# Kernel tuning notes

Measured on AMD Instinct MI355X. Metric: run time of the kernel, lower is better.

The kernel has to match this reference:

```python
import jax, jax.numpy as jnp
import numpy as np
from jax import lax

MAX_DISP = 4  # correlation window radius -> 9x9 = 81 offsets


def setup_inputs() -> dict:
    key = jax.random.key(0)
    k1, k2 = jax.random.split(key)
    B, C, H, W = 4, 256, 128, 128
    x_1 = jax.random.normal(k1, (B, C, H, W), dtype=jnp.float32)
    x_2 = jax.random.normal(k2, (B, C, H, W), dtype=jnp.float32)
    return {"x_1": x_1, "x_2": x_2}


def reference(x_1, x_2):
    # FlowNet-style correlation: for each displacement (dy, dx) in [-4, 4]^2,
    # out[b, (dy+4)*9 + (dx+4), y, x] = mean_c x1[b,c,y,x] * x2[b,c,y+dy,x+dx]
    # with zero padding of x2 (normalized by C, as in the original CUDA kernel).
    B, C, H, W = x_1.shape
    pad = jnp.pad(x_2, ((0, 0), (0, 0), (MAX_DISP, MAX_DISP), (MAX_DISP, MAX_DISP)))
    outs = []
    for dy in range(2 * MAX_DISP + 1):
        for dx in range(2 * MAX_DISP + 1):
            shifted = lax.dynamic_slice(pad, (0, 0, dy, dx), (B, C, H, W))
            outs.append(jnp.mean(x_1 * shifted, axis=1))  # [B, H, W]
    return jnp.stack(outs, axis=1)  # [B, 81, H, W]
```

## Files before the change

### kernel.cpp

```cpp
#include <hip/hip_runtime.h>
#include <stdint.h>


#define MD 4
constexpr int Bc = 4, Cc = 256, Hc = 128, Wc = 128;
constexpr int HW = Hc * Wc;
constexpr int TH = 16, TW = 16;
constexpr int CC = 4;
constexpr int SROWS = 18, SCOLS = 24;
constexpr int X2_SLOTS = CC * SROWS * (SCOLS / 4);
constexpr int X2_PAD   = 448;
constexpr int X1_SLOTS = CC * TH * (TW / 4);
constexpr int SL_TOT   = 768;
constexpr int BUF_DW   = SL_TOT * 4;
constexpr int X1OFF    = X2_PAD * 4;
constexpr int NTHR  = 192;
constexpr int NSLOT = 4;
constexpr int NK = Cc / CC;

__device__ __forceinline__ void async16(const void* g, const void* l) {
    __builtin_amdgcn_global_load_lds(
        (const __attribute__((address_space(1))) unsigned int*)g,
        (__attribute__((address_space(3))) unsigned int*)l, 16, 0, 0);
}

__global__ __launch_bounds__(NTHR, 2)
void corr_kernel(const float* __restrict__ x1, const float* __restrict__ x2,
                 const float* __restrict__ zpage, float* __restrict__ out)
{
    __shared__ float stg[3 * BUF_DW];

    const int tid  = threadIdx.x;
    const int w    = tid >> 6;
    const int lane = tid & 63;
    const int gy   = lane >> 2;
    const int gx   = lane & 3;

    const int bid = blockIdx.x;
    const int q   = bid / 24;
    const int r0  = bid - q * 24;
    const int g   = r0 >> 3;
    const int t   = q * 8 + (r0 & 7);
    const int tx = t & 7, ty = (t >> 3) & 7, bb = t >> 6;
    const int x0 = tx * TW, y0 = ty * TH;
    const int rowbase = y0 + 3 * g - MD;

    const char* sp[NSLOT];
    int sstep[NSLOT], sloff[NSLOT];
    const size_t cbase = (size_t)bb * Cc * HW;
    #pragma unroll
    for (int s = 0; s < NSLOT; ++s) {
        const int slot = tid + s * NTHR;
        sloff[s] = slot * 4;
        if (slot < X2_SLOTS) {
            const int cl  = slot / 108;
            const int rem = slot - cl * 108;
            const int rr  = rem / 6;
            const int gc  = rem - rr * 6;
            const int yy  = rowbase + rr;
            const int xx  = x0 - 4 + 4 * gc;
            const bool valid = ((unsigned)yy < (unsigned)Hc) && ((unsigned)xx <= (unsigned)(Wc - 4));
            sp[s]    = valid ? (const char*)(x2 + cbase + (size_t)cl * HW + yy * Wc + xx)
                             : (const char*)zpage;
            sstep[s] = valid ? (int)(CC * HW * sizeof(float)) : 0;
        } else if (slot < X2_PAD) {
            sp[s] = (const char*)zpage;  sstep[s] = 0;
        } else if (slot < X2_PAD + X1_SLOTS) {
            const int j   = slot - X2_PAD;
            const int cl  = j >> 6;
            const int py  = (j >> 2) & 15;
            const int pxg = j & 3;
            sp[s]    = (const char*)(x1 + cbase + (size_t)cl * HW + (y0 + py) * Wc + x0 + 4 * pxg);
            sstep[s] = (int)(CC * HW * sizeof(float));
        } else {
            sp[s] = (const char*)zpage;  sstep[s] = 0;
        }
    }

    float acc[9][4];
    #pragma unroll
    for (int dx = 0; dx < 9; ++dx)
        #pragma unroll
        for (int p = 0; p < 4; ++p) acc[dx][p] = 0.f;

    #pragma unroll
    for (int s = 0; s < NSLOT; ++s) {
        async16(sp[s], (const void*)(&stg[0 * BUF_DW] + sloff[s]));
        sp[s] += sstep[s];
    }
    #pragma unroll
    for (int s = 0; s < NSLOT; ++s) {
        async16(sp[s], (const void*)(&stg[1 * BUF_DW] + sloff[s]));
        sp[s] += sstep[s];
    }

    int bc = 0;
    for (int k = 0; k < NK; ++k) {
        if (k == NK - 1) __builtin_amdgcn_s_waitcnt(0x0F70);
        else             __builtin_amdgcn_s_waitcnt(0x0F74);
        __builtin_amdgcn_s_barrier();
        __builtin_amdgcn_sched_barrier(0);
        if (k + 2 < NK) {
            int b2 = bc + 2; if (b2 >= 3) b2 -= 3;
            float* bp2 = &stg[b2 * BUF_DW];
            #pragma unroll
            for (int s = 0; s < NSLOT; ++s) {
                async16(sp[s], (const void*)(bp2 + sloff[s]));
                sp[s] += sstep[s];
            }
        }
        const float* bp = &stg[bc * BUF_DW];
        #pragma unroll
        for (int cl = 0; cl < CC; ++cl) {
            const float4 a4 = *(const float4*)(bp + X1OFF + cl * 256 + gy * 16 + 4 * gx);
            const float* rowp = bp + cl * (SROWS * SCOLS) + (gy + w) * SCOLS + 4 * gx;
            const float4 q0 = *(const float4*)(rowp);
            const float4 q1 = *(const float4*)(rowp + 4);
            const float4 q2 = *(const float4*)(rowp + 8);
            const float v[12] = {q0.x, q0.y, q0.z, q0.w,
                                 q1.x, q1.y, q1.z, q1.w,
                                 q2.x, q2.y, q2.z, q2.w};
            const float a[4] = {a4.x, a4.y, a4.z, a4.w};
            #pragma unroll
            for (int dx = 0; dx < 9; ++dx)
                #pragma unroll
                for (int p = 0; p < 4; ++p)
                    acc[dx][p] += a[p] * v[dx + p];
        }
        if (++bc == 3) bc = 0;
    }

    const float inv = 1.0f / (float)Cc;
    float* ob = out + (((size_t)bb * 81 + (3 * g + w) * 9) * Hc + (y0 + gy)) * Wc + x0 + 4 * gx;
    #pragma unroll
    for (int dx = 0; dx < 9; ++dx) {
        float4 st = make_float4(acc[dx][0] * inv, acc[dx][1] * inv,
                                acc[dx][2] * inv, acc[dx][3] * inv);
        *(float4*)(ob + dx * HW) = st;
    }
}

extern "C" void kernel_launch(void* const* d_in, const int* in_sizes, int n_in,
                              void* d_out, int out_size, void* d_ws, size_t ws_size,
                              hipStream_t stream) {
    const float* x1 = (const float*)d_in[0];
    const float* x2 = (const float*)d_in[1];
    float* out = (float*)d_out;
    hipMemsetAsync(d_ws, 0, 64, stream);
    dim3 grid(3 * 8 * 8 * Bc), block(NTHR);
    corr_kernel<<<grid, block, 0, stream>>>(x1, x2, (const float*)d_ws, out);
}
```

Before: 204.2 us.

## Widen tiles to 32 columns, split channels in halves, and reduce with atomics

Tiles grow to 32x16 pixels with 8 outputs per thread, so each staged x2 row is reused across more outputs. The channel dimension is split across two blocks that combine partial sums with float atomicAdd into an output zeroed by a memset. x1 is now read straight from global memory instead of staged in LDS, and occupancy is raised to 3 blocks per SM. The costs are 72 accumulators per thread, a full-output memset, scalar atomic writes, and a summation order that is no longer deterministic.

```diff
diff --git a/kernel.cpp b/kernel.cpp
--- a/kernel.cpp
+++ b/kernel.cpp
@@ -5,26 +5,27 @@
 #define MD 4
 constexpr int Bc = 4, Cc = 256, Hc = 128, Wc = 128;
 constexpr int HW = Hc * Wc;
-constexpr int TH = 16, TW = 16;
+constexpr int TW = 32, TH = 16;
 constexpr int CC = 4;
-constexpr int SROWS = 18, SCOLS = 24;
-constexpr int X2_SLOTS = CC * SROWS * (SCOLS / 4);
-constexpr int X2_PAD   = 448;
-constexpr int X1_SLOTS = CC * TH * (TW / 4);
-constexpr int SL_TOT   = 768;
-constexpr int BUF_DW   = SL_TOT * 4;
-constexpr int X1OFF    = X2_PAD * 4;
-constexpr int NTHR  = 192;
-constexpr int NSLOT = 4;
-constexpr int NK = Cc / CC;
+constexpr int NK = 32;
+constexpr int SROWS = 18;
+constexpr int RSLOT = 11;
+constexpr int CH_SLOTS = SROWS * RSLOT;
+constexpr int REAL_SLOTS = CC * CH_SLOTS;
+constexpr int NTHR = 192;
+constexpr int NSLOT = 5;
+constexpr int SLOTS = NTHR * NSLOT;
+constexpr int BUF_DW = SLOTS * 4;
+constexpr int CH_DW = CH_SLOTS * 4;
+constexpr int ROW_DW = RSLOT * 4;
 
-__device__ __forceinline__ void async16(const void* g, const void* l) {
+__device__ __forceinline__ void async16(const void* g, void* l) {
     __builtin_amdgcn_global_load_lds(
         (const __attribute__((address_space(1))) unsigned int*)g,
         (__attribute__((address_space(3))) unsigned int*)l, 16, 0, 0);
 }
 
-__global__ __launch_bounds__(NTHR, 2)
+__global__ __launch_bounds__(NTHR, 3)
 void corr_kernel(const float* __restrict__ x1, const float* __restrict__ x2,
                  const float* __restrict__ zpage, float* __restrict__ out)
 {
@@ -34,109 +35,115 @@
     const int w    = tid >> 6;
     const int lane = tid & 63;
     const int gy   = lane >> 2;
-    const int gx   = lane & 3;
+    const int gxg  = lane & 3;
 
     const int bid = blockIdx.x;
-    const int q   = bid / 24;
-    const int r0  = bid - q * 24;
-    const int g   = r0 >> 3;
+    const int q   = bid / 48;
+    const int r0  = bid - q * 48;
+    const int sib = r0 >> 3;
     const int t   = q * 8 + (r0 & 7);
-    const int tx = t & 7, ty = (t >> 3) & 7, bb = t >> 6;
+    const int g   = sib % 3;
+    const int hf  = sib / 3;
+    const int tx = t & 3, ty = (t >> 2) & 7, bb = t >> 5;
     const int x0 = tx * TW, y0 = ty * TH;
     const int rowbase = y0 + 3 * g - MD;
 
+    const size_t cbase = ((size_t)bb * Cc + hf * 128) * HW;
+
     const char* sp[NSLOT];
     int sstep[NSLOT], sloff[NSLOT];
-    const size_t cbase = (size_t)bb * Cc * HW;
     #pragma unroll
     for (int s = 0; s < NSLOT; ++s) {
         const int slot = tid + s * NTHR;
         sloff[s] = slot * 4;
-        if (slot < X2_SLOTS) {
-            const int cl  = slot / 108;
-            const int rem = slot - cl * 108;
-            const int rr  = rem / 6;
-            const int gc  = rem - rr * 6;
-            const int yy  = rowbase + rr;
-            const int xx  = x0 - 4 + 4 * gc;
-            const bool valid = ((unsigned)yy < (unsigned)Hc) && ((unsigned)xx <= (unsigned)(Wc - 4));
-            sp[s]    = valid ? (const char*)(x2 + cbase + (size_t)cl * HW + yy * Wc + xx)
-                             : (const char*)zpage;
-            sstep[s] = valid ? (int)(CC * HW * sizeof(float)) : 0;
-        } else if (slot < X2_PAD) {
-            sp[s] = (const char*)zpage;  sstep[s] = 0;
-        } else if (slot < X2_PAD + X1_SLOTS) {
-            const int j   = slot - X2_PAD;
-            const int cl  = j >> 6;
-            const int py  = (j >> 2) & 15;
-            const int pxg = j & 3;
-            sp[s]    = (const char*)(x1 + cbase + (size_t)cl * HW + (y0 + py) * Wc + x0 + 4 * pxg);
-            sstep[s] = (int)(CC * HW * sizeof(float));
-        } else {
-            sp[s] = (const char*)zpage;  sstep[s] = 0;
+        const char* src = (const char*)zpage;
+        int step = 0;
+        if (slot < REAL_SLOTS) {
+            const int cl  = slot / CH_SLOTS;
+            const int rem = slot - cl * CH_SLOTS;
+            const int rr  = rem / RSLOT;
+            const int sl  = rem - rr * RSLOT;
+            if (sl < 10) {
+                const int yy = rowbase + rr;
+                const int xx = x0 - 4 + 4 * sl;
+                if ((unsigned)yy < (unsigned)Hc && (unsigned)xx <= (unsigned)(Wc - 4)) {
+                    src  = (const char*)(x2 + cbase + (size_t)cl * HW + yy * Wc + xx);
+                    step = (int)(CC * HW * sizeof(float));
+                }
+            }
         }
+        sp[s] = src;  sstep[s] = step;
     }
 
-    float acc[9][4];
+    const float* x1b = x1 + cbase + (y0 + gy) * Wc + x0 + 8 * gxg;
+
+    float acc[9][8];
     #pragma unroll
     for (int dx = 0; dx < 9; ++dx)
         #pragma unroll
-        for (int p = 0; p < 4; ++p) acc[dx][p] = 0.f;
+        for (int p = 0; p < 8; ++p) acc[dx][p] = 0.f;
 
     #pragma unroll
     for (int s = 0; s < NSLOT; ++s) {
-        async16(sp[s], (const void*)(&stg[0 * BUF_DW] + sloff[s]));
+        async16(sp[s], (void*)(&stg[0 * BUF_DW] + sloff[s]));
         sp[s] += sstep[s];
     }
     #pragma unroll
     for (int s = 0; s < NSLOT; ++s) {
-        async16(sp[s], (const void*)(&stg[1 * BUF_DW] + sloff[s]));
+        async16(sp[s], (void*)(&stg[1 * BUF_DW] + sloff[s]));
         sp[s] += sstep[s];
     }
 
     int bc = 0;
     for (int k = 0; k < NK; ++k) {
         if (k == NK - 1) __builtin_amdgcn_s_waitcnt(0x0F70);
-        else             __builtin_amdgcn_s_waitcnt(0x0F74);
+        else             __builtin_amdgcn_s_waitcnt(0x0F75);
         __builtin_amdgcn_s_barrier();
         __builtin_amdgcn_sched_barrier(0);
+
+        const float* bp = &stg[bc * BUF_DW];
+        #pragma unroll
+        for (int cl = 0; cl < CC; ++cl) {
+            const float* ap = x1b + (size_t)(k * CC + cl) * HW;
+            const float4 A0 = *(const float4*)(ap);
+            const float4 A1 = *(const float4*)(ap + 4);
+            const float* rowp = bp + cl * CH_DW + (gy + w) * ROW_DW + 8 * gxg;
+            const float4 q0 = *(const float4*)(rowp);
+            const float4 q1 = *(const float4*)(rowp + 4);
+            const float4 q2 = *(const float4*)(rowp + 8);
+            const float4 q3 = *(const float4*)(rowp + 12);
+            const float v[16] = {q0.x, q0.y, q0.z, q0.w, q1.x, q1.y, q1.z, q1.w,
+                                 q2.x, q2.y, q2.z, q2.w, q3.x, q3.y, q3.z, q3.w};
+            const float a[8] = {A0.x, A0.y, A0.z, A0.w, A1.x, A1.y, A1.z, A1.w};
+            #pragma unroll
+            for (int dx = 0; dx < 9; ++dx)
+                #pragma unroll
+                for (int p = 0; p < 8; ++p)
+                    acc[dx][p] += a[p] * v[p + dx];
+        }
+        __builtin_amdgcn_sched_barrier(0);
+
         if (k + 2 < NK) {
             int b2 = bc + 2; if (b2 >= 3) b2 -= 3;
             float* bp2 = &stg[b2 * BUF_DW];
             #pragma unroll
             for (int s = 0; s < NSLOT; ++s) {
-                async16(sp[s], (const void*)(bp2 + sloff[s]));
+                async16(sp[s], (void*)(bp2 + sloff[s]));
                 sp[s] += sstep[s];
             }
         }
-        const float* bp = &stg[bc * BUF_DW];
-        #pragma unroll
-        for (int cl = 0; cl < CC; ++cl) {
-            const float4 a4 = *(const float4*)(bp + X1OFF + cl * 256 + gy * 16 + 4 * gx);
-            const float* rowp = bp + cl * (SROWS * SCOLS) + (gy + w) * SCOLS + 4 * gx;
-            const float4 q0 = *(const float4*)(rowp);
-            const float4 q1 = *(const float4*)(rowp + 4);
-            const float4 q2 = *(const float4*)(rowp + 8);
-            const float v[12] = {q0.x, q0.y, q0.z, q0.w,
-                                 q1.x, q1.y, q1.z, q1.w,
-                                 q2.x, q2.y, q2.z, q2.w};
-            const float a[4] = {a4.x, a4.y, a4.z, a4.w};
-            #pragma unroll
-            for (int dx = 0; dx < 9; ++dx)
-                #pragma unroll
-                for (int p = 0; p < 4; ++p)
-                    acc[dx][p] += a[p] * v[dx + p];
-        }
+        __builtin_amdgcn_sched_barrier(0);
         if (++bc == 3) bc = 0;
     }
 
     const float inv = 1.0f / (float)Cc;
-    float* ob = out + (((size_t)bb * 81 + (3 * g + w) * 9) * Hc + (y0 + gy)) * Wc + x0 + 4 * gx;
+    float* ob = out + (((size_t)bb * 81 + (3 * g + w) * 9) * Hc + (y0 + gy)) * Wc + x0 + 8 * gxg;
     #pragma unroll
     for (int dx = 0; dx < 9; ++dx) {
-        float4 st = make_float4(acc[dx][0] * inv, acc[dx][1] * inv,
-                                acc[dx][2] * inv, acc[dx][3] * inv);
-        *(float4*)(ob + dx * HW) = st;
+        float* od = ob + (size_t)dx * HW;
+        #pragma unroll
+        for (int p = 0; p < 8; ++p)
+            atomicAdd(od + p, acc[dx][p] * inv);
     }
 }
 
@@ -146,7 +153,8 @@
     const float* x1 = (const float*)d_in[0];
     const float* x2 = (const float*)d_in[1];
     float* out = (float*)d_out;
+    hipMemsetAsync(d_out, 0, (size_t)out_size * sizeof(float), stream);
     hipMemsetAsync(d_ws, 0, 64, stream);
-    dim3 grid(3 * 8 * 8 * Bc), block(NTHR);
+    dim3 grid(4 * 8 * 4 * 6), block(NTHR);
     corr_kernel<<<grid, block, 0, stream>>>(x1, x2, (const float*)d_ws, out);
 }
```

Result: slower. 525.2 us (+157.3%).
